# Performance work log

Hardware: AMD Instinct MI355X
Metric: run time of the kernel (lower is better)

## Reference

```python
import jax, jax.numpy as jnp
import numpy as np

N = 100000          # nodes
E = 1600000         # edges (before self-loops)
F_IN = 128          # raw node features
TOPO = 8            # topological feature dim
HEADS1, HID1 = 8, 8 # conv1: 8 heads x 8 channels, concat -> 64
C_OUT = 40          # classes (conv2: 1 head, no concat)
NEG_SLOPE = 0.2     # PyG GATConv leaky_relu slope


def setup_inputs() -> dict:
    key = jax.random.key(0)
    ks = jax.random.split(key, 12)
    x = jax.random.normal(ks[0], (N, F_IN), jnp.float32)
    topo = jax.random.normal(ks[1], (N, TOPO), jnp.float32)
    edge_index = jax.random.randint(ks[2], (2, E), 0, N, jnp.int32)
    s = 0.1
    W1 = jax.random.normal(ks[3], (F_IN + TOPO, HEADS1 * HID1), jnp.float32) * s
    a_src1 = jax.random.normal(ks[4], (HEADS1, HID1), jnp.float32) * s
    a_dst1 = jax.random.normal(ks[5], (HEADS1, HID1), jnp.float32) * s
    b1 = jnp.zeros((HEADS1 * HID1,), jnp.float32)
    W2 = jax.random.normal(ks[6], (HEADS1 * HID1, C_OUT), jnp.float32) * s
    a_src2 = jax.random.normal(ks[7], (1, C_OUT), jnp.float32) * s
    a_dst2 = jax.random.normal(ks[8], (1, C_OUT), jnp.float32) * s
    b2 = jnp.zeros((C_OUT,), jnp.float32)
    return {"x": x, "topo": topo, "edge_index": edge_index,
            "W1": W1, "a_src1": a_src1, "a_dst1": a_dst1, "b1": b1,
            "W2": W2, "a_src2": a_src2, "a_dst2": a_dst2, "b2": b2}


def _gat_conv(x, src, dst, W, a_src, a_dst, b, heads, concat):
    # x: [N, Fin]; src/dst: [Etot] (self-loops already included)
    n = x.shape[0]
    h = (x @ W).reshape(n, heads, -1)                 # [N, H, C]
    alpha_s = jnp.sum(h * a_src[None], axis=-1)       # [N, H]
    alpha_d = jnp.sum(h * a_dst[None], axis=-1)       # [N, H]
    e = jax.nn.leaky_relu(alpha_s[src] + alpha_d[dst], NEG_SLOPE)  # [Etot, H]
    # segment softmax over destination nodes (numerically stable)
    m = jax.ops.segment_max(e, dst, num_segments=n)   # [N, H]
    ex = jnp.exp(e - m[dst])
    z = jax.ops.segment_sum(ex, dst, num_segments=n)  # [N, H]
    alpha = ex / (z[dst] + 1e-16)                     # [Etot, H]
    out = jax.ops.segment_sum(h[src] * alpha[..., None], dst, num_segments=n)  # [N,H,C]
    out = out.reshape(n, -1) if concat else out.mean(axis=1)
    return out + b


def reference(x, topo, edge_index, W1, a_src1, a_dst1, b1, W2, a_src2, a_dst2, b2):
    n = x.shape[0]
    loops = jnp.arange(n, dtype=edge_index.dtype)
    src = jnp.concatenate([edge_index[0], loops])  # PyG add_self_loops=True
    dst = jnp.concatenate([edge_index[1], loops])
    h = jnp.concatenate([x, topo], axis=1)         # [N, F_IN + TOPO]
    # dropout is identity in eval mode
    h = jax.nn.elu(_gat_conv(h, src, dst, W1, a_src1, a_dst1, b1, HEADS1, True))
    logits = _gat_conv(h, src, dst, W2, a_src2, a_dst2, b2, 1, False)
    return jax.nn.log_softmax(logits, axis=1)
```

## Files before the change

kernel.cpp:

```cpp
#include <hip/hip_runtime.h>
#include <math.h>


#define NBUK_MAX 512
#define BIN_CHUNK 4096
#define BUK_CAP 4608

typedef unsigned short ushort_t;

__device__ inline unsigned int f2bf(float f) {
    unsigned int u = __float_as_uint(f);
    u += 0x7FFFu + ((u >> 16) & 1u);
    return u >> 16;
}
__device__ inline float bf_lo(unsigned int u) {
    return __uint_as_float(u << 16);
}
__device__ inline float bf_hi(unsigned int u) {
    return __uint_as_float(u & 0xFFFF0000u);
}
__device__ inline float lrelu_exp(float q) {
    return __expf(q >= 0.f ? q : 0.2f * q);
}

__device__ inline int wave_incl_scan(int v, int lane) {
    #pragma unroll
    for (int ofs = 1; ofs < 64; ofs <<= 1) {
        int t = __shfl_up(v, ofs);
        if (lane >= ofs) v += t;
    }
    return v;
}

__global__ __launch_bounds__(256) void k_bin(const int* __restrict__ src,
                                             const int* __restrict__ dst,
                                             int* __restrict__ gCursor,
                                             unsigned int* __restrict__ tmp,
                                             int E, int NBUK) {
    __shared__ int lcnt[NBUK_MAX];
    __shared__ int lcur[NBUK_MAX];
    int tid = threadIdx.x;
    int base = blockIdx.x * BIN_CHUNK;
    for (int i = tid; i < NBUK; i += 256) lcnt[i] = 0;
    __syncthreads();
    int d[16];
    #pragma unroll
    for (int q = 0; q < 4; q++) {
        int e = base + q * 1024 + 4 * tid;
        if (e + 3 < E) {
            int4 v = *(const int4*)&dst[e];
            d[4 * q + 0] = v.x; d[4 * q + 1] = v.y;
            d[4 * q + 2] = v.z; d[4 * q + 3] = v.w;
        } else {
            #pragma unroll
            for (int k = 0; k < 4; k++)
                d[4 * q + k] = (e + k < E) ? dst[e + k] : -1;
        }
    }
    #pragma unroll
    for (int k = 0; k < 16; k++)
        if (d[k] >= 0) atomicAdd(&lcnt[d[k] >> 8], 1);
    __syncthreads();
    for (int b = tid; b < NBUK; b += 256) {
        int c = lcnt[b];
        lcur[b] = c ? b * BUK_CAP + atomicAdd(&gCursor[b], c) : 0;
    }
    __syncthreads();
    #pragma unroll
    for (int q = 0; q < 4; q++) {
        int e = base + q * 1024 + 4 * tid;
        int s[4];
        if (e + 3 < E) {
            int4 v = *(const int4*)&src[e];
            s[0] = v.x; s[1] = v.y; s[2] = v.z; s[3] = v.w;
        } else {
            #pragma unroll
            for (int k = 0; k < 4; k++)
                s[k] = (e + k < E) ? src[e + k] : 0;
        }
        #pragma unroll
        for (int k = 0; k < 4; k++) {
            int dd = d[4 * q + k];
            if (dd >= 0) {
                int p = atomicAdd(&lcur[dd >> 8], 1);
                tmp[p] = ((unsigned int)s[k] << 8) | (unsigned int)(dd & 255);
            }
        }
    }
}

__global__ __launch_bounds__(512) void k_fill2(const unsigned int* __restrict__ tmp,
                                               const int* __restrict__ gCursor,
                                               int* __restrict__ rowptr,
                                               int* __restrict__ rowEnd,
                                               int* __restrict__ csr, int N) {
    __shared__ int cnt[256];
    __shared__ int cur[256];
    __shared__ int wsum[4];
    int b = blockIdx.x, tid = threadIdx.x;
    int e0 = b * BUK_CAP;
    int cnt_e = gCursor[b];
    int e1 = e0 + cnt_e;
    if (tid < 256) cnt[tid] = 0;
    __syncthreads();
    {
        int nq = cnt_e >> 2;
        const uint4* t4 = (const uint4*)(tmp + e0);
        for (int q = tid; q < nq; q += 512) {
            uint4 v = t4[q];
            atomicAdd(&cnt[v.x & 255u], 1);
            atomicAdd(&cnt[v.y & 255u], 1);
            atomicAdd(&cnt[v.z & 255u], 1);
            atomicAdd(&cnt[v.w & 255u], 1);
        }
        for (int i = (nq << 2) + tid; i < cnt_e; i += 512)
            atomicAdd(&cnt[tmp[e0 + i] & 255u], 1);
    }
    __syncthreads();
    if (tid < 256) {
        int lane = tid & 63, wv = tid >> 6;
        int v = cnt[tid];
        int incl = wave_incl_scan(v, lane);
        if (lane == 63) wsum[wv] = incl;
        cnt[tid] = incl - v;
    }
    __syncthreads();
    if (tid < 256) {
        int wv = tid >> 6;
        int woff = 0;
        for (int i = 0; i < wv; i++) woff += wsum[i];
        int excl = woff + cnt[tid];
        int node = b * 256 + tid;
        int start = e0 + excl;
        cur[tid] = start;
        if (node < N) {
            rowptr[node] = start;
        }
    }
    __syncthreads();
    if (tid < 256) {
        int node = b * 256 + tid;
        if (node < N) rowEnd[node] = (tid < 255) ? cur[tid + 1] : e1;
    }
    __syncthreads();
    for (int i = e0 + tid; i < e1; i += 512) {
        unsigned int t = tmp[i];
        int p = atomicAdd(&cur[t & 255u], 1);
        csr[p] = (int)(t >> 8);
    }
}

__global__ __launch_bounds__(256) void k_xform1(const float* __restrict__ x,
                                                const float* __restrict__ topo,
                                                const float* __restrict__ W1,
                                                const float* __restrict__ asrc,
                                                const float* __restrict__ adst,
                                                ushort_t* __restrict__ h1b,
                                                float* __restrict__ as1,
                                                float* __restrict__ ad1, int N) {
    __shared__ float XT[136 * 64];
    int tid = threadIdx.x;
    int n0 = blockIdx.x * 64;
    {
        const float4* x4 = (const float4*)x;
        for (int i = tid; i < 2048; i += 256) {
            int node = i & 63, k4 = i >> 6;
            int gn = n0 + node; if (gn > N - 1) gn = N - 1;
            float4 v = x4[(size_t)gn * 32 + k4];
            int k = k4 * 4;
            XT[(k + 0) * 64 + node] = v.x;
            XT[(k + 1) * 64 + node] = v.y;
            XT[(k + 2) * 64 + node] = v.z;
            XT[(k + 3) * 64 + node] = v.w;
        }
        const float4* t4 = (const float4*)topo;
        if (tid < 128) {
            int node = tid & 63, j4 = tid >> 6;
            int gn = n0 + node; if (gn > N - 1) gn = N - 1;
            float4 v = t4[(size_t)gn * 2 + j4];
            int k = 128 + j4 * 4;
            XT[(k + 0) * 64 + node] = v.x;
            XT[(k + 1) * 64 + node] = v.y;
            XT[(k + 2) * 64 + node] = v.z;
            XT[(k + 3) * 64 + node] = v.w;
        }
    }
    __syncthreads();
    int ci = tid & 15, ni = tid >> 4;
    int nb = ni * 4, cb = ci * 4;
    const float4* Wp = (const float4*)&W1[cb];
    float acc[16];
    #pragma unroll
    for (int i = 0; i < 16; i++) acc[i] = 0.f;
    #pragma unroll 4
    for (int k = 0; k < 136; k++) {
        float4 xv = *(const float4*)&XT[k * 64 + nb];
        float4 wv = Wp[k * 16];
        acc[0]  = fmaf(xv.x, wv.x, acc[0]);  acc[1]  = fmaf(xv.x, wv.y, acc[1]);
        acc[2]  = fmaf(xv.x, wv.z, acc[2]);  acc[3]  = fmaf(xv.x, wv.w, acc[3]);
        acc[4]  = fmaf(xv.y, wv.x, acc[4]);  acc[5]  = fmaf(xv.y, wv.y, acc[5]);
        acc[6]  = fmaf(xv.y, wv.z, acc[6]);  acc[7]  = fmaf(xv.y, wv.w, acc[7]);
        acc[8]  = fmaf(xv.z, wv.x, acc[8]);  acc[9]  = fmaf(xv.z, wv.y, acc[9]);
        acc[10] = fmaf(xv.z, wv.z, acc[10]); acc[11] = fmaf(xv.z, wv.w, acc[11]);
        acc[12] = fmaf(xv.w, wv.x, acc[12]); acc[13] = fmaf(xv.w, wv.y, acc[13]);
        acc[14] = fmaf(xv.w, wv.z, acc[14]); acc[15] = fmaf(xv.w, wv.w, acc[15]);
    }
    int head = cb >> 3;
    #pragma unroll
    for (int i = 0; i < 4; i++) {
        int n = n0 + nb + i;
        unsigned int p0 = f2bf(acc[i * 4 + 0]) | (f2bf(acc[i * 4 + 1]) << 16);
        unsigned int p1 = f2bf(acc[i * 4 + 2]) | (f2bf(acc[i * 4 + 3]) << 16);
        if (n < N) *(uint2*)&h1b[(size_t)n * 64 + cb] = make_uint2(p0, p1);
        float s = 0.f, d = 0.f;
        #pragma unroll
        for (int j = 0; j < 4; j++) {
            s = fmaf(acc[i * 4 + j], asrc[cb + j], s);
            d = fmaf(acc[i * 4 + j], adst[cb + j], d);
        }
        s += __shfl_xor(s, 1);
        d += __shfl_xor(d, 1);
        if ((ci & 1) == 0 && n < N) {
            as1[n * 8 + head] = s;
            ad1[n * 8 + head] = d;
        }
    }
}

#define AGG_FMA(W_, U_)                                           \
    {                                                             \
        acc[0] = fmaf(W_, bf_lo(U_.x), acc[0]);                   \
        acc[1] = fmaf(W_, bf_hi(U_.x), acc[1]);                   \
        acc[2] = fmaf(W_, bf_lo(U_.y), acc[2]);                   \
        acc[3] = fmaf(W_, bf_hi(U_.y), acc[3]);                   \
        acc[4] = fmaf(W_, bf_lo(U_.z), acc[4]);                   \
        acc[5] = fmaf(W_, bf_hi(U_.z), acc[5]);                   \
        acc[6] = fmaf(W_, bf_lo(U_.w), acc[6]);                   \
        acc[7] = fmaf(W_, bf_hi(U_.w), acc[7]);                   \
        z += W_;                                                  \
    }

#define AGG1_GATHER(EIDX, SE_, AV_, UU_)                                     \
    int SE_ = __shfl(cv, nbase + ((EIDX) < d ? (EIDX) : dm1));               \
    SE_ = d > 0 ? SE_ : 0;                                                   \
    float AV_ = as1[SE_ * 8 + head];                                         \
    uint4 UU_ = *(const uint4*)(h1c + (((unsigned)SE_ << 7) + hoff));

#define AGG1_COMP(EIDX, AV_, UU_)                                            \
    {                                                                        \
        float w_ = (EIDX) < d ? lrelu_exp(AV_ + adv) : 0.f;                  \
        AGG_FMA(w_, UU_);                                                    \
    }

__global__ __launch_bounds__(256) void k_agg1(const ushort_t* __restrict__ h1b,
                                              const float* __restrict__ as1,
                                              const float* __restrict__ ad1,
                                              const float* __restrict__ b1,
                                              const int* __restrict__ rowptr,
                                              const int* __restrict__ rowEnd,
                                              const int* __restrict__ csr,
                                              float* __restrict__ h2, int N) {
    int tid = threadIdx.x, lane = tid & 63;
    int nbase0 = blockIdx.x * 8 + ((tid >> 6) << 1);
    if (nbase0 >= N) return;
    int nid = lane >> 5;
    int nbase = nid << 5;
    int l32 = lane & 31;
    int g = (lane >> 3) & 3;
    int head = lane & 7;
    int n = nbase0 + nid;
    bool valid = n < N;
    int nc = valid ? n : N - 1;
    const char* h1c = (const char*)h1b;
    unsigned hoff = (unsigned)head << 4;
    float adv = ad1[nc * 8 + head];
    float acc[8];
    #pragma unroll
    for (int k = 0; k < 8; k++) acc[k] = 0.f;
    float z = 0.f;

    int j0 = rowptr[nc], j1 = rowEnd[nc];
    int d = valid ? (j1 - j0) : 0;
    int dm1 = d > 0 ? d - 1 : 0;
    int dx = __shfl_xor(d, 32);
    int dmax = d > dx ? d : dx;
    int cv = csr[j0 + (l32 < d ? l32 : dm1)];

    {
        float w = lrelu_exp(as1[nc * 8 + head] + adv);
        if (g == 0 && valid) {
            uint4 u = *(const uint4*)(h1c + (((unsigned)nc << 7) + hoff));
            acc[0] = w * bf_lo(u.x); acc[1] = w * bf_hi(u.x);
            acc[2] = w * bf_lo(u.y); acc[3] = w * bf_hi(u.y);
            acc[4] = w * bf_lo(u.z); acc[5] = w * bf_hi(u.z);
            acc[6] = w * bf_lo(u.w); acc[7] = w * bf_hi(u.w);
            z = w;
        }
    }
    if (dmax > 0) {
        int e0 = g, e1 = 4 + g, e2 = 8 + g, e3 = 12 + g, e4 = 16 + g, e5 = 20 + g;
        AGG1_GATHER(e0, s0, a0, u0)
        AGG1_GATHER(e1, s1, a1, u1)
        AGG1_GATHER(e2, s2, a2, u2)
        AGG1_GATHER(e3, s3, a3, u3)
        AGG1_GATHER(e4, s4, a4, u4)
        AGG1_GATHER(e5, s5, a5, u5)
        AGG1_COMP(e0, a0, u0)
        if (dmax > 4)  AGG1_COMP(e1, a1, u1)
        if (dmax > 8)  AGG1_COMP(e2, a2, u2)
        if (dmax > 12) AGG1_COMP(e3, a3, u3)
        if (dmax > 16) AGG1_COMP(e4, a4, u4)
        if (dmax > 20) AGG1_COMP(e5, a5, u5)
        if (dmax > 24) {
            int e6 = 24 + g, e7 = 28 + g;
            AGG1_GATHER(e6, s6, a6, u6)
            AGG1_GATHER(e7, s7, a7, u7)
            AGG1_COMP(e6, a6, u6)
            if (dmax > 28) AGG1_COMP(e7, a7, u7)
            if (dmax > 32) {
                for (int eb = 32; eb < dmax; eb += 4) {
                    int e = eb + g;
                    int idx = e < d ? e : dm1;
                    int se = csr[j0 + idx];
                    se = d > 0 ? se : 0;
                    float av = as1[se * 8 + head];
                    uint4 u = *(const uint4*)(h1c + (((unsigned)se << 7) + hoff));
                    float w = e < d ? lrelu_exp(av + adv) : 0.f;
                    AGG_FMA(w, u);
                }
            }
        }
    }
    #pragma unroll
    for (int k = 0; k < 8; k++) {
        acc[k] += __shfl_xor(acc[k], 8);
        acc[k] += __shfl_xor(acc[k], 16);
    }
    z += __shfl_xor(z, 8); z += __shfl_xor(z, 16);
    if (g == 0 && valid) {
        float inv = 1.f / (z + 1e-16f);
        float o[8];
        #pragma unroll
        for (int k = 0; k < 8; k++) {
            float v = acc[k] * inv + b1[head * 8 + k];
            o[k] = v > 0.f ? v : (__expf(v) - 1.f);
        }
        float4* dp = (float4*)&h2[(size_t)n * 64 + head * 8];
        dp[0] = make_float4(o[0], o[1], o[2], o[3]);
        dp[1] = make_float4(o[4], o[5], o[6], o[7]);
    }
}

__global__ __launch_bounds__(256) void k_xform2(const float* __restrict__ h2,
                                                const float* __restrict__ W2,
                                                const float* __restrict__ asrc2,
                                                const float* __restrict__ adst2,
                                                ushort_t* __restrict__ gb,
                                                float* __restrict__ as2,
                                                float* __restrict__ ad2, int N) {
    __shared__ float XT[64 * 64];
    __shared__ float WS[64 * 40];
    int tid = threadIdx.x;
    int n0 = blockIdx.x * 64;
    {
        const float4* W4 = (const float4*)W2;
        float4* WS4 = (float4*)WS;
        for (int i = tid; i < 640; i += 256) WS4[i] = W4[i];
    }
    {
        const float4* h4 = (const float4*)h2;
        for (int i = tid; i < 1024; i += 256) {
            int node = i & 63, k4 = i >> 6;
            int gn = n0 + node; if (gn > N - 1) gn = N - 1;
            float4 v = h4[(size_t)gn * 16 + k4];
            int k = k4 * 4;
            XT[(k + 0) * 64 + node] = v.x;
            XT[(k + 1) * 64 + node] = v.y;
            XT[(k + 2) * 64 + node] = v.z;
            XT[(k + 3) * 64 + node] = v.w;
        }
    }
    __syncthreads();
    int ci = tid & 15, ni = tid >> 4;
    int nb = ni * 4, cb = ci * 4;
    float acc[16];
    #pragma unroll
    for (int i = 0; i < 16; i++) acc[i] = 0.f;
    if (ci < 10) {
        #pragma unroll 4
        for (int k = 0; k < 64; k++) {
            float4 xv = *(const float4*)&XT[k * 64 + nb];
            float4 wv = *(const float4*)&WS[k * 40 + cb];
            acc[0]  = fmaf(xv.x, wv.x, acc[0]);  acc[1]  = fmaf(xv.x, wv.y, acc[1]);
            acc[2]  = fmaf(xv.x, wv.z, acc[2]);  acc[3]  = fmaf(xv.x, wv.w, acc[3]);
            acc[4]  = fmaf(xv.y, wv.x, acc[4]);  acc[5]  = fmaf(xv.y, wv.y, acc[5]);
            acc[6]  = fmaf(xv.y, wv.z, acc[6]);  acc[7]  = fmaf(xv.y, wv.w, acc[7]);
            acc[8]  = fmaf(xv.z, wv.x, acc[8]);  acc[9]  = fmaf(xv.z, wv.y, acc[9]);
            acc[10] = fmaf(xv.z, wv.z, acc[10]); acc[11] = fmaf(xv.z, wv.w, acc[11]);
            acc[12] = fmaf(xv.w, wv.x, acc[12]); acc[13] = fmaf(xv.w, wv.y, acc[13]);
            acc[14] = fmaf(xv.w, wv.z, acc[14]); acc[15] = fmaf(xv.w, wv.w, acc[15]);
        }
    }
    #pragma unroll
    for (int i = 0; i < 4; i++) {
        int n = n0 + nb + i;
        if (ci < 10 && n < N) {
            unsigned int p0 = f2bf(acc[i * 4 + 0]) | (f2bf(acc[i * 4 + 1]) << 16);
            unsigned int p1 = f2bf(acc[i * 4 + 2]) | (f2bf(acc[i * 4 + 3]) << 16);
            *(uint2*)&gb[(size_t)n * 40 + cb] = make_uint2(p0, p1);
        }
        float s = 0.f, d = 0.f;
        if (ci < 10) {
            #pragma unroll
            for (int j = 0; j < 4; j++) {
                s = fmaf(acc[i * 4 + j], asrc2[cb + j], s);
                d = fmaf(acc[i * 4 + j], adst2[cb + j], d);
            }
        }
        s += __shfl_xor(s, 1); s += __shfl_xor(s, 2);
        s += __shfl_xor(s, 4); s += __shfl_xor(s, 8);
        d += __shfl_xor(d, 1); d += __shfl_xor(d, 2);
        d += __shfl_xor(d, 4); d += __shfl_xor(d, 8);
        if (ci == 0 && n < N) { as2[n] = s; ad2[n] = d; }
    }
}

#define AGG2_G(C_, SE_, AV_, UU_)                                            \
    int ee##C_ = 3 * (C_) + gg;                                              \
    int SE_ = __shfl(cv, nbase + (ee##C_ < d ? ee##C_ : dm1));               \
    SE_ = d > 0 ? SE_ : 0;                                                   \
    float AV_ = as2[SE_];                                                    \
    uint2 UU_ = *(const uint2*)(gbc + (unsigned)SE_ * 80u + poff);

#define AGG2_K(C_, AV_, UU_)                                                 \
    {                                                                        \
        float w_ = (ee##C_ < d) ? lrelu_exp(AV_ + add) : 0.f;                \
        acc[0] = fmaf(w_, bf_lo(UU_.x), acc[0]);                             \
        acc[1] = fmaf(w_, bf_hi(UU_.x), acc[1]);                             \
        acc[2] = fmaf(w_, bf_lo(UU_.y), acc[2]);                             \
        acc[3] = fmaf(w_, bf_hi(UU_.y), acc[3]);                             \
        z += w_;                                                             \
    }

__global__ __launch_bounds__(256) void k_agg2(const ushort_t* __restrict__ gb,
                                              const float* __restrict__ as2,
                                              const float* __restrict__ ad2,
                                              const float* __restrict__ b2,
                                              const int* __restrict__ rowptr,
                                              const int* __restrict__ rowEnd,
                                              const int* __restrict__ csr,
                                              float* __restrict__ out, int N) {
    int tid = threadIdx.x, lane = tid & 63;
    int nbase0 = blockIdx.x * 8 + ((tid >> 6) << 1);
    if (nbase0 >= N) return;
    int nid = lane >> 5;
    int nbase = nid << 5;
    int l32 = lane & 31;
    int gg = l32 / 10;
    int p = l32 - gg * 10;
    if (gg > 2) { gg = 2; p = 9; }
    int n = nbase0 + nid;
    bool valid = n < N;
    int nc = valid ? n : N - 1;
    const char* gbc = (const char*)gb;
    unsigned poff = (unsigned)p << 3;
    float add = ad2[nc];
    float acc[4] = {0.f, 0.f, 0.f, 0.f};
    float z = 0.f;

    int j0 = rowptr[nc], j1 = rowEnd[nc];
    int d = valid ? (j1 - j0) : 0;
    int dm1 = d > 0 ? d - 1 : 0;
    int dxx = __shfl_xor(d, 32);
    int dmax = d > dxx ? d : dxx;
    int cv = csr[j0 + (l32 < d ? l32 : dm1)];

    {
        float w = lrelu_exp(as2[nc] + add);
        if (gg == 0 && valid) {
            uint2 u = *(const uint2*)(gbc + (unsigned)nc * 80u + poff);
            acc[0] = w * bf_lo(u.x); acc[1] = w * bf_hi(u.x);
            acc[2] = w * bf_lo(u.y); acc[3] = w * bf_hi(u.y);
            z = w;
        }
    }
    if (dmax > 0) {
        AGG2_G(0, s0, a0, u0)
        AGG2_G(1, s1, a1, u1)
        AGG2_G(2, s2, a2, u2)
        AGG2_G(3, s3, a3, u3)
        AGG2_G(4, s4, a4, u4)
        AGG2_G(5, s5, a5, u5)
        AGG2_G(6, s6, a6, u6)
        AGG2_G(7, s7, a7, u7)
        AGG2_K(0, a0, u0)
        if (dmax > 3)  AGG2_K(1, a1, u1)
        if (dmax > 6)  AGG2_K(2, a2, u2)
        if (dmax > 9)  AGG2_K(3, a3, u3)
        if (dmax > 12) AGG2_K(4, a4, u4)
        if (dmax > 15) AGG2_K(5, a5, u5)
        if (dmax > 18) AGG2_K(6, a6, u6)
        if (dmax > 21) AGG2_K(7, a7, u7)
        if (dmax > 24) {
            AGG2_G(8, s8, a8, u8)
            AGG2_G(9, s9, a9, u9)
            AGG2_K(8, a8, u8)
            if (dmax > 27) AGG2_K(9, a9, u9)
            if (dmax > 30) {
                for (int eb = 30; eb < dmax; eb += 3) {
                    int e = eb + gg;
                    int idx = e < d ? e : dm1;
                    int se = csr[j0 + idx];
                    se = d > 0 ? se : 0;
                    float av = as2[se];
                    uint2 u = *(const uint2*)(gbc + (unsigned)se * 80u + poff);
                    float w = (e < d) ? lrelu_exp(av + add) : 0.f;
                    acc[0] = fmaf(w, bf_lo(u.x), acc[0]);
                    acc[1] = fmaf(w, bf_hi(u.x), acc[1]);
                    acc[2] = fmaf(w, bf_lo(u.y), acc[2]);
                    acc[3] = fmaf(w, bf_hi(u.y), acc[3]);
                    z += w;
                }
            }
        }
    }
    #pragma unroll
    for (int k = 0; k < 4; k++) {
        float t1 = __shfl(acc[k], lane + 10);
        float t2 = __shfl(acc[k], lane + 20);
        acc[k] += t1 + t2;
    }
    {
        float t1 = __shfl(z, lane + 10);
        float t2 = __shfl(z, lane + 20);
        z += t1 + t2;
    }
    bool act = (l32 < 10) && valid;
    float l[4];
    float mv = -INFINITY;
    if (act) {
        float inv = 1.f / (z + 1e-16f);
        #pragma unroll
        for (int k = 0; k < 4; k++) {
            l[k] = acc[k] * inv + b2[p * 4 + k];
            mv = fmaxf(mv, l[k]);
        }
    }
    mv = fmaxf(mv, __shfl_xor(mv, 1));
    mv = fmaxf(mv, __shfl_xor(mv, 2));
    mv = fmaxf(mv, __shfl_xor(mv, 4));
    mv = fmaxf(mv, __shfl_xor(mv, 8));
    float ev = 0.f;
    if (act) {
        #pragma unroll
        for (int k = 0; k < 4; k++) ev += __expf(l[k] - mv);
    }
    ev += __shfl_xor(ev, 1);
    ev += __shfl_xor(ev, 2);
    ev += __shfl_xor(ev, 4);
    ev += __shfl_xor(ev, 8);
    if (act) {
        float ls = mv + __logf(ev);
        float4* dp = (float4*)&out[(size_t)n * 40 + p * 4];
        dp[0] = make_float4(l[0] - ls, l[1] - ls, l[2] - ls, l[3] - ls);
    }
}

extern "C" void kernel_launch(void* const* d_in, const int* in_sizes, int n_in,
                              void* d_out, int out_size, void* d_ws, size_t ws_size,
                              hipStream_t stream) {
    const float* x    = (const float*)d_in[0];
    const float* topo = (const float*)d_in[1];
    const int*   ei   = (const int*)d_in[2];
    const float* W1   = (const float*)d_in[3];
    const float* a_s1 = (const float*)d_in[4];
    const float* a_d1 = (const float*)d_in[5];
    const float* b1   = (const float*)d_in[6];
    const float* W2   = (const float*)d_in[7];
    const float* a_s2 = (const float*)d_in[8];
    const float* a_d2 = (const float*)d_in[9];
    const float* b2   = (const float*)d_in[10];
    float* out = (float*)d_out;

    int N = in_sizes[0] / 128;
    int E = in_sizes[2] / 2;
    const int* esrc = ei;
    const int* edst = ei + E;
    int NBUK = (N + 255) / 256;
    size_t cap = (size_t)NBUK * BUK_CAP;

    char* ws = (char*)d_ws;
    size_t off = 0;
    auto alloc = [&](size_t bytes) -> void* {
        void* p = ws + off;
        off = (off + bytes + 255) & ~(size_t)255;
        return p;
    };
    ushort_t* h1b  = (ushort_t*)alloc((size_t)N * 64 * 2);
    float* as1     = (float*)alloc((size_t)N * 8 * 4);
    float* ad1     = (float*)alloc((size_t)N * 8 * 4);
    float* h2      = (float*)alloc((size_t)N * 64 * 4);
    ushort_t* gb   = (ushort_t*)alloc((size_t)N * 40 * 2);
    float* as2     = (float*)alloc((size_t)N * 4);
    float* ad2     = (float*)alloc((size_t)N * 4);
    int*   rowptr  = (int*)alloc((size_t)N * 4);
    int*   rowEnd  = (int*)alloc((size_t)N * 4);
    int*   csr     = (int*)alloc(cap * 4);
    unsigned int* tmp = (unsigned int*)alloc(cap * 4);
    int* gCursor   = (int*)alloc((size_t)NBUK * 4);

    hipMemsetAsync(gCursor, 0, (size_t)NBUK * 4, stream);
    int nbin = (E + BIN_CHUNK - 1) / BIN_CHUNK;
    k_bin<<<nbin, 256, 0, stream>>>(esrc, edst, gCursor, tmp, E, NBUK);
    k_fill2<<<NBUK, 512, 0, stream>>>(tmp, gCursor, rowptr, rowEnd, csr, N);

    int nbg = (N + 63) / 64;
    int nb8 = (N + 7) / 8;
    k_xform1<<<nbg, 256, 0, stream>>>(x, topo, W1, a_s1, a_d1, h1b, as1, ad1, N);
    k_agg1<<<nb8, 256, 0, stream>>>(h1b, as1, ad1, b1, rowptr, rowEnd, csr, h2, N);
    k_xform2<<<nbg, 256, 0, stream>>>(h2, W2, a_s2, a_d2, gb, as2, ad2, N);
    k_agg2<<<nb8, 256, 0, stream>>>(gb, as2, ad2, b2, rowptr, rowEnd, csr, out, N);
}
```

Measured before the change: 283.0 us.

## Compute conv1 feature transform with bf16 MFMA instead of scalar FP32 FMA

Rewrites the first-layer X·W1 projection kernel to stage node features and W1 into shared memory as bf16, padded to K=160, and runs the product with 16x16x32 bf16 MFMA instructions, one wave per 16-node tile. The attention projections are reduced with lane shuffles over the MFMA output layout. The aim is to remove scalar FMA compute cost from this stage. In exchange, inputs are rounded to bf16 before the matmul, every block re-converts W1 and writes transposed into LDS, and h1 is now stored as scattered 2-byte writes instead of packed 8-byte writes.

Result: faster. 271.4 us (-4.1%).

```diff
diff --git a/kernel.cpp b/kernel.cpp
--- a/kernel.cpp
+++ b/kernel.cpp
@@ -7,6 +7,8 @@
 #define BUK_CAP 4608
 
 typedef unsigned short ushort_t;
+typedef short bf16x8 __attribute__((ext_vector_type(8)));
+typedef float f32x4 __attribute__((ext_vector_type(4)));
 
 __device__ inline unsigned int f2bf(float f) {
     unsigned int u = __float_as_uint(f);
@@ -158,71 +160,80 @@
                                                 ushort_t* __restrict__ h1b,
                                                 float* __restrict__ as1,
                                                 float* __restrict__ ad1, int N) {
-    __shared__ float XT[136 * 64];
+    __shared__ ushort_t XA[64 * 168];
+    __shared__ ushort_t WB[64 * 168];
+    unsigned int* XAu = (unsigned int*)XA;
+    unsigned int* WBu = (unsigned int*)WB;
     int tid = threadIdx.x;
     int n0 = blockIdx.x * 64;
+    const float4* x4 = (const float4*)x;
+    for (int i = tid; i < 2048; i += 256) {
+        int nd = i >> 5, q = i & 31;
+        int gn = n0 + nd; if (gn > N - 1) gn = N - 1;
+        float4 v = x4[(size_t)gn * 32 + q];
+        XAu[nd * 84 + 2 * q]     = f2bf(v.x) | (f2bf(v.y) << 16);
+        XAu[nd * 84 + 2 * q + 1] = f2bf(v.z) | (f2bf(v.w) << 16);
+    }
+    const float4* t4 = (const float4*)topo;
+    for (int i = tid; i < 128; i += 256) {
+        int nd = i >> 1, q = i & 1;
+        int gn = n0 + nd; if (gn > N - 1) gn = N - 1;
+        float4 v = t4[(size_t)gn * 2 + q];
+        XAu[nd * 84 + 64 + 2 * q]     = f2bf(v.x) | (f2bf(v.y) << 16);
+        XAu[nd * 84 + 64 + 2 * q + 1] = f2bf(v.z) | (f2bf(v.w) << 16);
+    }
+    for (int i = tid; i < 1024; i += 256) {
+        int nd = i >> 4, q = i & 15;
+        XAu[nd * 84 + 68 + q] = 0;
+    }
     {
-        const float4* x4 = (const float4*)x;
-        for (int i = tid; i < 2048; i += 256) {
-            int node = i & 63, k4 = i >> 6;
-            int gn = n0 + node; if (gn > N - 1) gn = N - 1;
-            float4 v = x4[(size_t)gn * 32 + k4];
-            int k = k4 * 4;
-            XT[(k + 0) * 64 + node] = v.x;
-            XT[(k + 1) * 64 + node] = v.y;
-            XT[(k + 2) * 64 + node] = v.z;
-            XT[(k + 3) * 64 + node] = v.w;
-        }
-        const float4* t4 = (const float4*)topo;
-        if (tid < 128) {
-            int node = tid & 63, j4 = tid >> 6;
-            int gn = n0 + node; if (gn > N - 1) gn = N - 1;
-            float4 v = t4[(size_t)gn * 2 + j4];
-            int k = 128 + j4 * 4;
-            XT[(k + 0) * 64 + node] = v.x;
-            XT[(k + 1) * 64 + node] = v.y;
-            XT[(k + 2) * 64 + node] = v.z;
-            XT[(k + 3) * 64 + node] = v.w;
-        }
-    }
-    __syncthreads();
-    int ci = tid & 15, ni = tid >> 4;
-    int nb = ni * 4, cb = ci * 4;
-    const float4* Wp = (const float4*)&W1[cb];
-    float acc[16];
-    #pragma unroll
-    for (int i = 0; i < 16; i++) acc[i] = 0.f;
-    #pragma unroll 4
-    for (int k = 0; k < 136; k++) {
-        float4 xv = *(const float4*)&XT[k * 64 + nb];
-        float4 wv = Wp[k * 16];
-        acc[0]  = fmaf(xv.x, wv.x, acc[0]);  acc[1]  = fmaf(xv.x, wv.y, acc[1]);
-        acc[2]  = fmaf(xv.x, wv.z, acc[2]);  acc[3]  = fmaf(xv.x, wv.w, acc[3]);
-        acc[4]  = fmaf(xv.y, wv.x, acc[4]);  acc[5]  = fmaf(xv.y, wv.y, acc[5]);
-        acc[6]  = fmaf(xv.y, wv.z, acc[6]);  acc[7]  = fmaf(xv.y, wv.w, acc[7]);
-        acc[8]  = fmaf(xv.z, wv.x, acc[8]);  acc[9]  = fmaf(xv.z, wv.y, acc[9]);
-        acc[10] = fmaf(xv.z, wv.z, acc[10]); acc[11] = fmaf(xv.z, wv.w, acc[11]);
-        acc[12] = fmaf(xv.w, wv.x, acc[12]); acc[13] = fmaf(xv.w, wv.y, acc[13]);
-        acc[14] = fmaf(xv.w, wv.z, acc[14]); acc[15] = fmaf(xv.w, wv.w, acc[15]);
-    }
-    int head = cb >> 3;
-    #pragma unroll
-    for (int i = 0; i < 4; i++) {
-        int n = n0 + nb + i;
-        unsigned int p0 = f2bf(acc[i * 4 + 0]) | (f2bf(acc[i * 4 + 1]) << 16);
-        unsigned int p1 = f2bf(acc[i * 4 + 2]) | (f2bf(acc[i * 4 + 3]) << 16);
-        if (n < N) *(uint2*)&h1b[(size_t)n * 64 + cb] = make_uint2(p0, p1);
-        float s = 0.f, d = 0.f;
+        int c = tid & 63;
+        for (int k = tid >> 6; k < 136; k += 4)
+            WB[c * 168 + k] = (ushort_t)f2bf(W1[k * 64 + c]);
+    }
+    for (int i = tid; i < 1024; i += 256) {
+        int c = i >> 4, q = i & 15;
+        WBu[c * 84 + 68 + q] = 0;
+    }
+    __syncthreads();
+    int w = tid >> 6, l = tid & 63;
+    int cl = l & 15;
+    int arow = (w << 4) + cl;
+    int kb0 = (l >> 4) << 3;
+    f32x4 acc0 = {0.f, 0.f, 0.f, 0.f};
+    f32x4 acc1 = acc0, acc2 = acc0, acc3 = acc0;
+    #pragma unroll
+    for (int ks = 0; ks < 5; ks++) {
+        int kb = kb0 + (ks << 5);
+        bf16x8 af = *(const bf16x8*)&XA[arow * 168 + kb];
+        bf16x8 b0 = *(const bf16x8*)&WB[(cl)      * 168 + kb];
+        bf16x8 b1 = *(const bf16x8*)&WB[(16 + cl) * 168 + kb];
+        bf16x8 b2 = *(const bf16x8*)&WB[(32 + cl) * 168 + kb];
+        bf16x8 b3 = *(const bf16x8*)&WB[(48 + cl) * 168 + kb];
+        acc0 = __builtin_amdgcn_mfma_f32_16x16x32_bf16(af, b0, acc0, 0, 0, 0);
+        acc1 = __builtin_amdgcn_mfma_f32_16x16x32_bf16(af, b1, acc1, 0, 0, 0);
+        acc2 = __builtin_amdgcn_mfma_f32_16x16x32_bf16(af, b2, acc2, 0, 0, 0);
+        acc3 = __builtin_amdgcn_mfma_f32_16x16x32_bf16(af, b3, acc3, 0, 0, 0);
+    }
+    int rbase = n0 + (w << 4) + ((l >> 4) << 2);
+    #pragma unroll
+    for (int nt = 0; nt < 4; nt++) {
+        f32x4 a = (nt == 0) ? acc0 : (nt == 1) ? acc1 : (nt == 2) ? acc2 : acc3;
+        int col = (nt << 4) + cl;
+        float asc = asrc[col], adc = adst[col];
         #pragma unroll
-        for (int j = 0; j < 4; j++) {
-            s = fmaf(acc[i * 4 + j], asrc[cb + j], s);
-            d = fmaf(acc[i * 4 + j], adst[cb + j], d);
-        }
-        s += __shfl_xor(s, 1);
-        d += __shfl_xor(d, 1);
-        if ((ci & 1) == 0 && n < N) {
-            as1[n * 8 + head] = s;
-            ad1[n * 8 + head] = d;
+        for (int r = 0; r < 4; r++) {
+            int n = rbase + r;
+            if (n < N) h1b[(size_t)n * 64 + col] = (ushort_t)f2bf(a[r]);
+            float s = a[r] * asc;
+            float dd = a[r] * adc;
+            s += __shfl_xor(s, 1); s += __shfl_xor(s, 2); s += __shfl_xor(s, 4);
+            dd += __shfl_xor(dd, 1); dd += __shfl_xor(dd, 2); dd += __shfl_xor(dd, 4);
+            if ((l & 7) == 0 && n < N) {
+                int head = col >> 3;
+                as1[n * 8 + head] = s;
+                ad1[n * 8 + head] = dd;
+            }
         }
     }
 }
```
